# Performance work log

Hardware: AMD Instinct MI355X
Metric: run time of the kernel (lower is better)

The kernel has to match this reference:

```python
import jax, jax.numpy as jnp
import numpy as np

DIM = 768
HEADS = 12
T_TOK = 4  # num_frames // tubelet_size
EPS = 1e-6


def _layernorm(x, w, b):
    m = jnp.mean(x, axis=-1, keepdims=True)
    v = jnp.var(x, axis=-1, keepdims=True)
    return (x - m) * jax.lax.rsqrt(v + EPS) * w + b


def _conv1d(g, w, b):
    # g: (Bv, C, T), w: (C_out, C_in, 3) torch layout, padding=1
    y = jax.lax.conv_general_dilated(g, w, window_strides=(1,), padding=[(1, 1)],
                                     dimension_numbers=("NCH", "OIH", "NCH"))
    return y + b[None, :, None]


def setup_inputs() -> dict:
    key = jax.random.key(0)
    ks = jax.random.split(key, 16)
    D, F = DIM, DIM * 4
    s = 0.02
    return {
        "x": jax.random.normal(ks[0], (64, 197, D), jnp.float32),
        "ln1_w": jnp.ones((D,), jnp.float32),
        "ln1_b": jnp.zeros((D,), jnp.float32),
        "qkv_w": jax.random.normal(ks[1], (3 * D, D), jnp.float32) * s,
        "qkv_b": jnp.zeros((3 * D,), jnp.float32),
        "convq_w": jax.random.normal(ks[2], (D, D, 3), jnp.float32) * s,
        "convq_b": jnp.zeros((D,), jnp.float32),
        "convk_w": jax.random.normal(ks[3], (D, D, 3), jnp.float32) * s,
        "convk_b": jnp.zeros((D,), jnp.float32),
        "proj_w": jax.random.normal(ks[4], (D, D), jnp.float32) * s,
        "proj_b": jnp.zeros((D,), jnp.float32),
        "ln2_w": jnp.ones((D,), jnp.float32),
        "ln2_b": jnp.zeros((D,), jnp.float32),
        "ff1_w": jax.random.normal(ks[5], (F, D), jnp.float32) * s,
        "ff1_b": jnp.zeros((F,), jnp.float32),
        "ff2_w": jax.random.normal(ks[6], (D, F), jnp.float32) * s,
        "ff2_b": jnp.zeros((D,), jnp.float32),
    }


def reference(x, ln1_w, ln1_b, qkv_w, qkv_b, convq_w, convq_b, convk_w, convk_b,
              proj_w, proj_b, ln2_w, ln2_b, ff1_w, ff1_b, ff2_w, ff2_b):
    B, N, C = x.shape
    H, Dh = HEADS, C // HEADS

    # --- attention branch ---
    h = _layernorm(x, ln1_w, ln1_b)
    # temporal context from per-frame CLS tokens
    g = h[:, 0, :].reshape(B // T_TOK, T_TOK, C).transpose(0, 2, 1)  # (Bv, C, T)
    cq = _conv1d(g, convq_w, convq_b).transpose(0, 2, 1).reshape(B, H, 1, Dh)
    ck = _conv1d(g, convk_w, convk_b).transpose(0, 2, 1).reshape(B, H, 1, Dh)

    qkv = (h @ qkv_w.T + qkv_b).reshape(B, N, 3, H, Dh).transpose(2, 0, 3, 1, 4)
    q, k, v = qkv[0], qkv[1], qkv[2]  # (B, H, N, Dh)

    scale = Dh ** -0.5
    scores = jnp.einsum("bhnd,bhmd->bhnm", q + cq, k + ck) * scale
    attn = jax.nn.softmax(scores, axis=-1)
    o = jnp.einsum("bhnm,bhmd->bhnd", attn, v)
    o = o.transpose(0, 2, 1, 3).reshape(B, N, C)
    o = o @ proj_w.T + proj_b
    x = x + o

    # --- FFN branch ---
    h2 = _layernorm(x, ln2_w, ln2_b)
    h2 = jax.nn.gelu(h2 @ ff1_w.T + ff1_b, approximate=False)
    x = x + (h2 @ ff2_w.T + ff2_b)
    return x
```

## Files before the change

kernel.cpp:

```cpp
#include <hip/hip_runtime.h>
#include <hip/hip_bf16.h>


typedef __attribute__((ext_vector_type(8))) short  short8;
typedef __attribute__((ext_vector_type(4))) float  float4v;
typedef __attribute__((ext_vector_type(4))) unsigned short ushort4v;

#define DEV static __device__ __forceinline__

DEV unsigned short f2bf(float f) {
  union { float f; unsigned u; } v; v.f = f;
  unsigned r = v.u + 0x7fffu + ((v.u >> 16) & 1u);
  return (unsigned short)(r >> 16);
}
DEV float bf2f(unsigned short h) {
  union { unsigned u; float f; } v; v.u = ((unsigned)h) << 16;
  return v.f;
}

DEV void gld_lds16(const void* g, void* l) {
  __builtin_amdgcn_global_load_lds(
      (const __attribute__((address_space(1))) void*)g,
      (__attribute__((address_space(3))) void*)l, 16, 0, 0);
}

__global__ void wcvt(const float* __restrict__ in, unsigned short* __restrict__ out, int n4) {
  int i = blockIdx.x * 256 + threadIdx.x;
  if (i >= n4) return;
  float4 f = *((const float4*)in + i);
  ushort4v o;
  o[0] = f2bf(f.x); o[1] = f2bf(f.y); o[2] = f2bf(f.z); o[3] = f2bf(f.w);
  *(ushort4v*)(out + (size_t)i * 4) = o;
}

__global__ __launch_bounds__(256) void ln_k(const float* __restrict__ x,
                                            const float* __restrict__ w,
                                            const float* __restrict__ b,
                                            unsigned short* __restrict__ out) {
  int row = blockIdx.x;
  size_t base = (size_t)row * 768;
  int tid = threadIdx.x;
  float v0 = x[base + tid], v1 = x[base + tid + 256], v2 = x[base + tid + 512];
  float s = v0 + v1 + v2;
  float q = v0 * v0 + v1 * v1 + v2 * v2;
  for (int m = 1; m < 64; m <<= 1) { s += __shfl_xor(s, m); q += __shfl_xor(q, m); }
  __shared__ float sh[8];
  int wid = tid >> 6, lane = tid & 63;
  if (lane == 0) { sh[wid] = s; sh[4 + wid] = q; }
  __syncthreads();
  s = sh[0] + sh[1] + sh[2] + sh[3];
  q = sh[4] + sh[5] + sh[6] + sh[7];
  float mean = s * (1.f / 768.f);
  float var  = q * (1.f / 768.f) - mean * mean;
  float rstd = rsqrtf(var + 1e-6f);
  out[base + tid      ] = f2bf((v0 - mean) * rstd * w[tid      ] + b[tid      ]);
  out[base + tid + 256] = f2bf((v1 - mean) * rstd * w[tid + 256] + b[tid + 256]);
  out[base + tid + 512] = f2bf((v2 - mean) * rstd * w[tid + 512] + b[tid + 512]);
}

__global__ __launch_bounds__(256) void conv_cls(const unsigned short* __restrict__ h,
                                                const float* __restrict__ wq,
                                                const float* __restrict__ wk,
                                                float* __restrict__ cq,
                                                float* __restrict__ ck) {
  __shared__ float gsh[16][6][48];
  int tid = threadIdx.x;
  int cc = blockIdx.x;
  int kc = blockIdx.y;
  for (int idx = tid; idx < 16 * 2 * 48; idx += 256) {
    int ci = idx % 48; int t = (idx / 48) & 1; int v = idx / 96;
    gsh[v][t * 5][ci] = 0.f;
  }
  for (int idx = tid; idx < 16 * 4 * 48; idx += 256) {
    int ci = idx % 48; int t = (idx / 48) & 3; int v = idx / 192;
    gsh[v][t + 1][ci] = bf2f(h[(size_t)(v * 4 + t) * 197 * 768 + kc * 48 + ci]);
  }
  __syncthreads();
  int cl = tid >> 2, t = tid & 3;
  int cout = cc * 64 + cl;
  const float* wqp = wq + ((size_t)cout * 768 + kc * 48) * 3;
  const float* wkp = wk + ((size_t)cout * 768 + kc * 48) * 3;
  float aq[16] = {}, ak[16] = {};
  for (int ci = 0; ci < 48; ++ci) {
    float q0 = wqp[ci * 3], q1 = wqp[ci * 3 + 1], q2 = wqp[ci * 3 + 2];
    float k0 = wkp[ci * 3], k1 = wkp[ci * 3 + 1], k2 = wkp[ci * 3 + 2];
#pragma unroll
    for (int v = 0; v < 16; ++v) {
      float g0 = gsh[v][t][ci], g1 = gsh[v][t + 1][ci], g2 = gsh[v][t + 2][ci];
      aq[v] += q0 * g0 + q1 * g1 + q2 * g2;
      ak[v] += k0 * g0 + k1 * g1 + k2 * g2;
    }
  }
#pragma unroll
  for (int v = 0; v < 16; ++v) {
    atomicAdd(&cq[(size_t)(v * 4 + t) * 768 + cout], aq[v]);
    atomicAdd(&ck[(size_t)(v * 4 + t) * 768 + cout], ak[v]);
  }
}

template <int EPI>
__global__ __launch_bounds__(256, 2) void gemm_k(
    const unsigned short* __restrict__ A, const unsigned short* __restrict__ W,
    int M, int N, int K, const float* __restrict__ bias,
    float* __restrict__ out_f, unsigned short* __restrict__ out_h,
    const float* __restrict__ res,
    const float* __restrict__ cq, const float* __restrict__ ck,
    const float* __restrict__ cqb, const float* __restrict__ ckb,
    unsigned short* __restrict__ Qo, unsigned short* __restrict__ Ko,
    unsigned short* __restrict__ Vo) {
  __shared__ unsigned short As[128 * 32];
  __shared__ unsigned short Bs[128 * 32];
  int tid = threadIdx.x;
  int wid = tid >> 6, lane = tid & 63;
  int wr = wid >> 1, wc = wid & 1;
  int cG = lane >> 4, cl = lane & 15;
  long rowBase = (long)blockIdx.x * 128;
  int colBase = blockIdx.y * 128;

  float4v acc[4][4] = {};

  int off0 = tid * 16, off1 = (256 + tid) * 16;
  int r0s = off0 >> 6, r1s = off1 >> 6;
  int s0 = (off0 >> 4) & 3, s1 = (off1 >> 4) & 3;
  int k0s = (s0 ^ ((r0s >> 1) & 3)) * 8;
  int k1s = (s1 ^ ((r1s >> 1) & 3)) * 8;
  long ar0 = rowBase + r0s; if (ar0 > M - 1) ar0 = M - 1;
  long ar1 = rowBase + r1s; if (ar1 > M - 1) ar1 = M - 1;
  const unsigned short* a0 = A + ar0 * K + k0s;
  const unsigned short* a1 = A + ar1 * K + k1s;
  const unsigned short* w0 = W + (long)(colBase + r0s) * K + k0s;
  const unsigned short* w1 = W + (long)(colBase + r1s) * K + k1s;

  for (int kt = 0; kt < K; kt += 32) {
    __syncthreads();
    gld_lds16(a0 + kt, As + (off0 >> 1));
    gld_lds16(a1 + kt, As + (off1 >> 1));
    gld_lds16(w0 + kt, Bs + (off0 >> 1));
    gld_lds16(w1 + kt, Bs + (off1 >> 1));
    __syncthreads();
    short8 af[4], bfr[4];
#pragma unroll
    for (int fi = 0; fi < 4; ++fi) {
      int r = wr * 64 + fi * 16 + cl;
      int sl = cG ^ ((r >> 1) & 3);
      af[fi] = *(const short8*)(As + r * 32 + sl * 8);
    }
#pragma unroll
    for (int fj = 0; fj < 4; ++fj) {
      int r = wc * 64 + fj * 16 + cl;
      int sl = cG ^ ((r >> 1) & 3);
      bfr[fj] = *(const short8*)(Bs + r * 32 + sl * 8);
    }
#pragma unroll
    for (int fi = 0; fi < 4; ++fi)
#pragma unroll
      for (int fj = 0; fj < 4; ++fj)
        acc[fi][fj] = __builtin_amdgcn_mfma_f32_16x16x32_bf16(af[fi], bfr[fj], acc[fi][fj], 0, 0, 0);
  }

#pragma unroll
  for (int fi = 0; fi < 4; ++fi) {
    long r0 = rowBase + wr * 64 + fi * 16 + 4 * cG;
#pragma unroll
    for (int fj = 0; fj < 4; ++fj) {
      int col = colBase + wc * 64 + fj * 16 + cl;
      float bc = bias[col];
      float4v a = acc[fi][fj];
#pragma unroll
      for (int j = 0; j < 4; ++j) {
        long row = r0 + j;
        if (row >= M) continue;
        float v = a[j] + bc;
        if constexpr (EPI == 0) {
          int sec = col / 768; int ccc = col - sec * 768;
          int bi = (int)(row / 197); int ni = (int)(row - (long)bi * 197);
          size_t oidx = ((size_t)(bi * 12 + (ccc >> 6)) * 197 + ni) * 64 + (ccc & 63);
          if (sec == 0)      { v += cq[bi * 768 + ccc] + cqb[ccc]; Qo[oidx] = f2bf(v); }
          else if (sec == 1) { v += ck[bi * 768 + ccc] + ckb[ccc]; Ko[oidx] = f2bf(v); }
          else               { Vo[oidx] = f2bf(v); }
        } else if constexpr (EPI == 1 || EPI == 3) {
          size_t idx = (size_t)row * N + col;
          out_f[idx] = v + res[idx];
        } else {
          size_t idx = (size_t)row * N + col;
          float g = 0.5f * v * (1.0f + erff(v * 0.70710678118f));
          out_h[idx] = f2bf(g);
        }
      }
    }
  }
}

__global__ __launch_bounds__(256, 2) void attn_k(const unsigned short* __restrict__ Q,
                                                 const unsigned short* __restrict__ Kg,
                                                 const unsigned short* __restrict__ Vg,
                                                 unsigned short* __restrict__ O) {
  __shared__ unsigned short Ks[224 * 64];
  __shared__ unsigned short Vt[64 * 224];
  __shared__ unsigned short Ps[4][16 * 40];
  int g = blockIdx.x;
  int bi = g / 12, hh = g - bi * 12;
  size_t gbase = (size_t)g * 197 * 64;
  int tid = threadIdx.x, wid = tid >> 6, lane = tid & 63;
  int cG = lane >> 4, cl = lane & 15;

  {
    int rr = tid >> 3, ch = tid & 7;
#pragma unroll
    for (int i = 0; i < 7; ++i) {
      int n = rr + 32 * i;
      short8 kv = {0, 0, 0, 0, 0, 0, 0, 0};
      if (n < 197) kv = *(const short8*)(Kg + gbase + (size_t)n * 64 + ch * 8);
      *(short8*)(Ks + n * 64 + (ch ^ (n & 7)) * 8) = kv;
      short8 vv = {0, 0, 0, 0, 0, 0, 0, 0};
      if (n < 197) vv = *(const short8*)(Vg + gbase + (size_t)n * 64 + ch * 8);
#pragma unroll
      for (int j = 0; j < 8; ++j) {
        int dd = ch * 8 + j;
        Vt[dd * 224 + (n ^ ((dd & 7) << 3))] = ((unsigned short*)&vv)[j];
      }
    }
  }
  __syncthreads();

  for (int rt = wid; rt < 13; rt += 4) {
    int nq = rt * 16 + cl; if (nq > 196) nq = 196;
    short8 aq0 = *(const short8*)(Q + gbase + (size_t)nq * 64 + 8 * cG);
    short8 aq1 = *(const short8*)(Q + gbase + (size_t)nq * 64 + 32 + 8 * cG);
    float4v s[14];
#pragma unroll
    for (int ct = 0; ct < 14; ++ct) {
      float4v a = {0.f, 0.f, 0.f, 0.f};
      int np = ct * 16 + cl;
      short8 b0 = *(const short8*)(Ks + np * 64 + ((cG    ) ^ (np & 7)) * 8);
      short8 b1 = *(const short8*)(Ks + np * 64 + ((4 + cG) ^ (np & 7)) * 8);
      a = __builtin_amdgcn_mfma_f32_16x16x32_bf16(aq0, b0, a, 0, 0, 0);
      a = __builtin_amdgcn_mfma_f32_16x16x32_bf16(aq1, b1, a, 0, 0, 0);
      s[ct] = a;
    }
    float mx[4] = {-1e30f, -1e30f, -1e30f, -1e30f};
#pragma unroll
    for (int ct = 0; ct < 14; ++ct) {
      int colv = ct * 16 + cl;
#pragma unroll
      for (int j = 0; j < 4; ++j) {
        float v = (colv < 197) ? s[ct][j] * 0.125f : -1e30f;
        s[ct][j] = v;
        mx[j] = fmaxf(mx[j], v);
      }
    }
#pragma unroll
    for (int m = 1; m < 16; m <<= 1)
#pragma unroll
      for (int j = 0; j < 4; ++j) mx[j] = fmaxf(mx[j], __shfl_xor(mx[j], m));
    float sum[4] = {0.f, 0.f, 0.f, 0.f};
#pragma unroll
    for (int ct = 0; ct < 14; ++ct)
#pragma unroll
      for (int j = 0; j < 4; ++j) {
        float p = __expf(s[ct][j] - mx[j]);
        s[ct][j] = p;
        sum[j] += p;
      }
#pragma unroll
    for (int m = 1; m < 16; m <<= 1)
#pragma unroll
      for (int j = 0; j < 4; ++j) sum[j] += __shfl_xor(sum[j], m);
    float rs[4];
#pragma unroll
    for (int j = 0; j < 4; ++j) rs[j] = 1.0f / sum[j];

    float4v oa[4] = {};
    unsigned short* P = &Ps[wid][0];
#pragma unroll
    for (int ks = 0; ks < 7; ++ks) {
#pragma unroll
      for (int t = 0; t < 2; ++t) {
        int ct = 2 * ks + t;
#pragma unroll
        for (int j = 0; j < 4; ++j)
          P[(4 * cG + j) * 40 + t * 16 + cl] = f2bf(s[ct][j]);
      }
      short8 pa = *(const short8*)(P + cl * 40 + 8 * cG);
#pragma unroll
      for (int dt = 0; dt < 4; ++dt) {
        int dd = dt * 16 + cl;
        short8 bv = *(const short8*)(Vt + dd * 224 + ((ks * 32 + 8 * cG) ^ ((dd & 7) << 3)));
        oa[dt] = __builtin_amdgcn_mfma_f32_16x16x32_bf16(pa, bv, oa[dt], 0, 0, 0);
      }
    }
#pragma unroll
    for (int dt = 0; dt < 4; ++dt)
#pragma unroll
      for (int j = 0; j < 4; ++j) {
        int n2 = rt * 16 + 4 * cG + j;
        if (n2 < 197)
          O[(size_t)(bi * 197 + n2) * 768 + hh * 64 + dt * 16 + cl] = f2bf(oa[dt][j] * rs[j]);
      }
  }
}

extern "C" void kernel_launch(void* const* d_in, const int* in_sizes, int n_in,
                              void* d_out, int out_size, void* d_ws, size_t ws_size,
                              hipStream_t stream) {
  const float* x     = (const float*)d_in[0];
  const float* ln1w  = (const float*)d_in[1];
  const float* ln1b  = (const float*)d_in[2];
  const float* qkvw  = (const float*)d_in[3];
  const float* qkvb  = (const float*)d_in[4];
  const float* cqw   = (const float*)d_in[5];
  const float* cqb   = (const float*)d_in[6];
  const float* ckw   = (const float*)d_in[7];
  const float* ckb   = (const float*)d_in[8];
  const float* projw = (const float*)d_in[9];
  const float* projb = (const float*)d_in[10];
  const float* ln2w  = (const float*)d_in[11];
  const float* ln2b  = (const float*)d_in[12];
  const float* ff1w  = (const float*)d_in[13];
  const float* ff1b  = (const float*)d_in[14];
  const float* ff2w  = (const float*)d_in[15];
  const float* ff2b  = (const float*)d_in[16];
  float* out = (float*)d_out;

  char* ws = (char*)d_ws;
  const size_t SZ = (size_t)12608 * 768 * 2;
  unsigned short* Qb  = (unsigned short*)(ws);
  unsigned short* Kb  = (unsigned short*)(ws + SZ);
  unsigned short* Vb  = (unsigned short*)(ws + 2 * SZ);
  unsigned short* Ob  = (unsigned short*)(ws + 3 * SZ);
  unsigned short* ffh = (unsigned short*)(ws);
  unsigned short* hb  = (unsigned short*)(ws + 4 * SZ);
  float* x1 = (float*)(ws + 5 * SZ);
  float* cq = (float*)(ws + 5 * SZ + (size_t)12608 * 768 * 4);
  float* ck = cq + 49152;
  unsigned short* Wqkv  = (unsigned short*)(ck + 49152);
  unsigned short* Wproj = Wqkv + 1769472;
  unsigned short* Wff1  = Wproj + 589824;
  unsigned short* Wff2  = Wff1 + 2359296;

  wcvt<<<1728, 256, 0, stream>>>(qkvw, Wqkv, 442368);
  wcvt<<<576,  256, 0, stream>>>(projw, Wproj, 147456);
  wcvt<<<2304, 256, 0, stream>>>(ff1w, Wff1, 589824);
  wcvt<<<2304, 256, 0, stream>>>(ff2w, Wff2, 589824);

  ln_k<<<12608, 256, 0, stream>>>(x, ln1w, ln1b, hb);

  hipMemsetAsync(cq, 0, 2 * 49152 * sizeof(float), stream);
  conv_cls<<<dim3(12, 16), 256, 0, stream>>>(hb, cqw, ckw, cq, ck);

  gemm_k<0><<<dim3(99, 18), 256, 0, stream>>>(hb, Wqkv, 12608, 2304, 768, qkvb,
      nullptr, nullptr, nullptr, cq, ck, cqb, ckb, Qb, Kb, Vb);

  attn_k<<<768, 256, 0, stream>>>(Qb, Kb, Vb, Ob);

  gemm_k<1><<<dim3(99, 6), 256, 0, stream>>>(Ob, Wproj, 12608, 768, 768, projb,
      x1, nullptr, x, nullptr, nullptr, nullptr, nullptr, nullptr, nullptr, nullptr);

  ln_k<<<12608, 256, 0, stream>>>(x1, ln2w, ln2b, hb);

  gemm_k<2><<<dim3(99, 24), 256, 0, stream>>>(hb, Wff1, 12608, 3072, 768, ff1b,
      nullptr, ffh, nullptr, nullptr, nullptr, nullptr, nullptr, nullptr, nullptr, nullptr);

  gemm_k<3><<<dim3(99, 6), 256, 0, stream>>>(ffh, Wff2, 12608, 768, 3072, ff2b,
      out, nullptr, x1, nullptr, nullptr, nullptr, nullptr, nullptr, nullptr, nullptr);
}
```

Measured before the change: 624.5 us.

## Use 256x256 double-buffered GEMM tiles with XCD-aware scheduling and per-wave layernorm

The GEMM kernel goes from 128x128 tiles with K-step 32 and a single LDS buffer to 256x256 tiles with K-step 64 and double-buffered LDS, run by 512-thread blocks with 8 waves. The next tile is prefetched while the current one is multiplied, which removes one barrier per iteration and raises data reuse per load. Blocks are remapped by XCD so that neighbouring tiles share L2. LayerNorm now handles one row per wave with float4 loads and no shared-memory reduction. The cost is fewer blocks (150 for the N=768 GEMMs), which risks leaving CUs idle, plus 128KB of LDS per block, which likely limits occupancy to one block per CU despite launch_bounds(512,2).

```diff
diff --git a/kernel.cpp b/kernel.cpp
--- a/kernel.cpp
+++ b/kernel.cpp
@@ -5,15 +5,16 @@
 typedef __attribute__((ext_vector_type(8))) short  short8;
 typedef __attribute__((ext_vector_type(4))) float  float4v;
 typedef __attribute__((ext_vector_type(4))) unsigned short ushort4v;
+typedef unsigned short ushort;
 
 #define DEV static __device__ __forceinline__
 
-DEV unsigned short f2bf(float f) {
+DEV ushort f2bf(float f) {
   union { float f; unsigned u; } v; v.f = f;
   unsigned r = v.u + 0x7fffu + ((v.u >> 16) & 1u);
-  return (unsigned short)(r >> 16);
-}
-DEV float bf2f(unsigned short h) {
+  return (ushort)(r >> 16);
+}
+DEV float bf2f(ushort h) {
   union { unsigned u; float f; } v; v.u = ((unsigned)h) << 16;
   return v.f;
 }
@@ -24,7 +25,7 @@
       (__attribute__((address_space(3))) void*)l, 16, 0, 0);
 }
 
-__global__ void wcvt(const float* __restrict__ in, unsigned short* __restrict__ out, int n4) {
+__global__ void wcvt(const float* __restrict__ in, ushort* __restrict__ out, int n4) {
   int i = blockIdx.x * 256 + threadIdx.x;
   if (i >= n4) return;
   float4 f = *((const float4*)in + i);
@@ -36,29 +37,40 @@
 __global__ __launch_bounds__(256) void ln_k(const float* __restrict__ x,
                                             const float* __restrict__ w,
                                             const float* __restrict__ b,
-                                            unsigned short* __restrict__ out) {
-  int row = blockIdx.x;
+                                            ushort* __restrict__ out) {
+  int wid = threadIdx.x >> 6, lane = threadIdx.x & 63;
+  int row = blockIdx.x * 4 + wid;
   size_t base = (size_t)row * 768;
-  int tid = threadIdx.x;
-  float v0 = x[base + tid], v1 = x[base + tid + 256], v2 = x[base + tid + 512];
-  float s = v0 + v1 + v2;
-  float q = v0 * v0 + v1 * v1 + v2 * v2;
+  const float4* xr = (const float4*)(x + base);
+  const float4* w4 = (const float4*)w;
+  const float4* b4 = (const float4*)b;
+  float4 v[3];
+  float s = 0.f, q = 0.f;
+#pragma unroll
+  for (int j = 0; j < 3; ++j) {
+    v[j] = xr[j * 64 + lane];
+    s += v[j].x + v[j].y + v[j].z + v[j].w;
+    q += v[j].x * v[j].x + v[j].y * v[j].y + v[j].z * v[j].z + v[j].w * v[j].w;
+  }
+#pragma unroll
   for (int m = 1; m < 64; m <<= 1) { s += __shfl_xor(s, m); q += __shfl_xor(q, m); }
-  __shared__ float sh[8];
-  int wid = tid >> 6, lane = tid & 63;
-  if (lane == 0) { sh[wid] = s; sh[4 + wid] = q; }
-  __syncthreads();
-  s = sh[0] + sh[1] + sh[2] + sh[3];
-  q = sh[4] + sh[5] + sh[6] + sh[7];
   float mean = s * (1.f / 768.f);
   float var  = q * (1.f / 768.f) - mean * mean;
   float rstd = rsqrtf(var + 1e-6f);
-  out[base + tid      ] = f2bf((v0 - mean) * rstd * w[tid      ] + b[tid      ]);
-  out[base + tid + 256] = f2bf((v1 - mean) * rstd * w[tid + 256] + b[tid + 256]);
-  out[base + tid + 512] = f2bf((v2 - mean) * rstd * w[tid + 512] + b[tid + 512]);
-}
-
-__global__ __launch_bounds__(256) void conv_cls(const unsigned short* __restrict__ h,
+  ushort* orow = out + base;
+#pragma unroll
+  for (int j = 0; j < 3; ++j) {
+    float4 wv = w4[j * 64 + lane], bv = b4[j * 64 + lane];
+    ushort4v o;
+    o[0] = f2bf((v[j].x - mean) * rstd * wv.x + bv.x);
+    o[1] = f2bf((v[j].y - mean) * rstd * wv.y + bv.y);
+    o[2] = f2bf((v[j].z - mean) * rstd * wv.z + bv.z);
+    o[3] = f2bf((v[j].w - mean) * rstd * wv.w + bv.w);
+    *(ushort4v*)(orow + (size_t)(j * 64 + lane) * 4) = o;
+  }
+}
+
+__global__ __launch_bounds__(256) void conv_cls(const ushort* __restrict__ h,
                                                 const float* __restrict__ wq,
                                                 const float* __restrict__ wk,
                                                 float* __restrict__ cq,
@@ -99,68 +111,92 @@
 }
 
 template <int EPI>
-__global__ __launch_bounds__(256, 2) void gemm_k(
-    const unsigned short* __restrict__ A, const unsigned short* __restrict__ W,
-    int M, int N, int K, const float* __restrict__ bias,
-    float* __restrict__ out_f, unsigned short* __restrict__ out_h,
+__global__ __launch_bounds__(512, 2) void gemm256(
+    const ushort* __restrict__ A, const ushort* __restrict__ W,
+    int M, int N, int K, int mt, const float* __restrict__ bias,
+    float* __restrict__ out_f, ushort* __restrict__ out_h,
     const float* __restrict__ res,
     const float* __restrict__ cq, const float* __restrict__ ck,
     const float* __restrict__ cqb, const float* __restrict__ ckb,
-    unsigned short* __restrict__ Qo, unsigned short* __restrict__ Ko,
-    unsigned short* __restrict__ Vo) {
-  __shared__ unsigned short As[128 * 32];
-  __shared__ unsigned short Bs[128 * 32];
+    ushort* __restrict__ Qo, ushort* __restrict__ Ko, ushort* __restrict__ Vo) {
+  __shared__ ushort As[2][256 * 64];
+  __shared__ ushort Bs[2][256 * 64];
+
+  int nwg = gridDim.x;
+  int bid = blockIdx.x;
+  int q8 = nwg >> 3, r8 = nwg & 7;
+  int xcd = bid & 7, idx = bid >> 3;
+  int wg = (xcd < r8 ? xcd * (q8 + 1) : r8 * (q8 + 1) + (xcd - r8) * q8) + idx;
+  int tileCol = wg / mt;
+  int tileRow = wg - tileCol * mt;
+
+  long rowBase = (long)tileRow * 256;
+  int  colBase = tileCol * 256;
+
   int tid = threadIdx.x;
   int wid = tid >> 6, lane = tid & 63;
-  int wr = wid >> 1, wc = wid & 1;
+  int wr = wid >> 2, wc = wid & 3;
   int cG = lane >> 4, cl = lane & 15;
-  long rowBase = (long)blockIdx.x * 128;
-  int colBase = blockIdx.y * 128;
-
-  float4v acc[4][4] = {};
-
-  int off0 = tid * 16, off1 = (256 + tid) * 16;
-  int r0s = off0 >> 6, r1s = off1 >> 6;
-  int s0 = (off0 >> 4) & 3, s1 = (off1 >> 4) & 3;
-  int k0s = (s0 ^ ((r0s >> 1) & 3)) * 8;
-  int k1s = (s1 ^ ((r1s >> 1) & 3)) * 8;
-  long ar0 = rowBase + r0s; if (ar0 > M - 1) ar0 = M - 1;
-  long ar1 = rowBase + r1s; if (ar1 > M - 1) ar1 = M - 1;
-  const unsigned short* a0 = A + ar0 * K + k0s;
-  const unsigned short* a1 = A + ar1 * K + k1s;
-  const unsigned short* w0 = W + (long)(colBase + r0s) * K + k0s;
-  const unsigned short* w1 = W + (long)(colBase + r1s) * K + k1s;
-
-  for (int kt = 0; kt < K; kt += 32) {
+
+  const ushort* asrc[4];
+  const ushort* wsrc[4];
+  int dstoff[4];
+#pragma unroll
+  for (int j = 0; j < 4; ++j) {
+    int flat = j * 512 + tid;
+    int r = flat >> 3, c = flat & 7;
+    long ar = rowBase + r; if (ar > M - 1) ar = M - 1;
+    asrc[j] = A + ar * (size_t)K + (c ^ (r & 7)) * 8;
+    wsrc[j] = W + (size_t)(colBase + r) * K + (c ^ (r & 7)) * 8;
+    dstoff[j] = flat * 8;
+  }
+
+  float4v acc[8][4] = {};
+
+#pragma unroll
+  for (int j = 0; j < 4; ++j) {
+    gld_lds16(asrc[j], &As[0][0] + dstoff[j]);
+    gld_lds16(wsrc[j], &Bs[0][0] + dstoff[j]);
+  }
+  __syncthreads();
+
+  int nt = K >> 6;
+  for (int t = 0; t < nt; ++t) {
+    const ushort* as = &As[t & 1][0];
+    const ushort* bs = &Bs[t & 1][0];
+    if (t + 1 < nt) {
+      ushort* an = &As[(t + 1) & 1][0];
+      ushort* bn = &Bs[(t + 1) & 1][0];
+      int kt = (t + 1) << 6;
+#pragma unroll
+      for (int j = 0; j < 4; ++j) {
+        gld_lds16(asrc[j] + kt, an + dstoff[j]);
+        gld_lds16(wsrc[j] + kt, bn + dstoff[j]);
+      }
+    }
+#pragma unroll
+    for (int ks = 0; ks < 2; ++ks) {
+      short8 bfv[4];
+#pragma unroll
+      for (int fj = 0; fj < 4; ++fj) {
+        int r = wc * 64 + fj * 16 + cl;
+        bfv[fj] = *(const short8*)(bs + r * 64 + (((ks << 2) | cG) ^ (r & 7)) * 8);
+      }
+#pragma unroll
+      for (int fi = 0; fi < 8; ++fi) {
+        int r = wr * 128 + fi * 16 + cl;
+        short8 av = *(const short8*)(as + r * 64 + (((ks << 2) | cG) ^ (r & 7)) * 8);
+#pragma unroll
+        for (int fj = 0; fj < 4; ++fj)
+          acc[fi][fj] = __builtin_amdgcn_mfma_f32_16x16x32_bf16(av, bfv[fj], acc[fi][fj], 0, 0, 0);
+      }
+    }
     __syncthreads();
-    gld_lds16(a0 + kt, As + (off0 >> 1));
-    gld_lds16(a1 + kt, As + (off1 >> 1));
-    gld_lds16(w0 + kt, Bs + (off0 >> 1));
-    gld_lds16(w1 + kt, Bs + (off1 >> 1));
-    __syncthreads();
-    short8 af[4], bfr[4];
-#pragma unroll
-    for (int fi = 0; fi < 4; ++fi) {
-      int r = wr * 64 + fi * 16 + cl;
-      int sl = cG ^ ((r >> 1) & 3);
-      af[fi] = *(const short8*)(As + r * 32 + sl * 8);
-    }
-#pragma unroll
-    for (int fj = 0; fj < 4; ++fj) {
-      int r = wc * 64 + fj * 16 + cl;
-      int sl = cG ^ ((r >> 1) & 3);
-      bfr[fj] = *(const short8*)(Bs + r * 32 + sl * 8);
-    }
-#pragma unroll
-    for (int fi = 0; fi < 4; ++fi)
-#pragma unroll
-      for (int fj = 0; fj < 4; ++fj)
-        acc[fi][fj] = __builtin_amdgcn_mfma_f32_16x16x32_bf16(af[fi], bfr[fj], acc[fi][fj], 0, 0, 0);
-  }
-
-#pragma unroll
-  for (int fi = 0; fi < 4; ++fi) {
-    long r0 = rowBase + wr * 64 + fi * 16 + 4 * cG;
+  }
+
+#pragma unroll
+  for (int fi = 0; fi < 8; ++fi) {
+    long r0 = rowBase + wr * 128 + fi * 16 + 4 * cG;
 #pragma unroll
     for (int fj = 0; fj < 4; ++fj) {
       int col = colBase + wc * 64 + fj * 16 + cl;
@@ -191,13 +227,13 @@
   }
 }
 
-__global__ __launch_bounds__(256, 2) void attn_k(const unsigned short* __restrict__ Q,
-                                                 const unsigned short* __restrict__ Kg,
-                                                 const unsigned short* __restrict__ Vg,
-                                                 unsigned short* __restrict__ O) {
-  __shared__ unsigned short Ks[224 * 64];
-  __shared__ unsigned short Vt[64 * 224];
-  __shared__ unsigned short Ps[4][16 * 40];
+__global__ __launch_bounds__(256, 2) void attn_k(const ushort* __restrict__ Q,
+                                                 const ushort* __restrict__ Kg,
+                                                 const ushort* __restrict__ Vg,
+                                                 ushort* __restrict__ O) {
+  __shared__ ushort Ks[224 * 64];
+  __shared__ ushort Vt[64 * 224];
+  __shared__ ushort Ps[4][16 * 40];
   int g = blockIdx.x;
   int bi = g / 12, hh = g - bi * 12;
   size_t gbase = (size_t)g * 197 * 64;
@@ -217,7 +253,7 @@
 #pragma unroll
       for (int j = 0; j < 8; ++j) {
         int dd = ch * 8 + j;
-        Vt[dd * 224 + (n ^ ((dd & 7) << 3))] = ((unsigned short*)&vv)[j];
+        Vt[dd * 224 + (n ^ ((dd & 7) << 3))] = ((ushort*)&vv)[j];
       }
     }
   }
@@ -271,7 +307,7 @@
     for (int j = 0; j < 4; ++j) rs[j] = 1.0f / sum[j];
 
     float4v oa[4] = {};
-    unsigned short* P = &Ps[wid][0];
+    ushort* P = &Ps[wid][0];
 #pragma unroll
     for (int ks = 0; ks < 7; ++ks) {
 #pragma unroll
@@ -324,43 +360,43 @@
 
   char* ws = (char*)d_ws;
   const size_t SZ = (size_t)12608 * 768 * 2;
-  unsigned short* Qb  = (unsigned short*)(ws);
-  unsigned short* Kb  = (unsigned short*)(ws + SZ);
-  unsigned short* Vb  = (unsigned short*)(ws + 2 * SZ);
-  unsigned short* Ob  = (unsigned short*)(ws + 3 * SZ);
-  unsigned short* ffh = (unsigned short*)(ws);
-  unsigned short* hb  = (unsigned short*)(ws + 4 * SZ);
+  ushort* Qb  = (ushort*)(ws);
+  ushort* Kb  = (ushort*)(ws + SZ);
+  ushort* Vb  = (ushort*)(ws + 2 * SZ);
+  ushort* Ob  = (ushort*)(ws + 3 * SZ);
+  ushort* ffh = (ushort*)(ws);
+  ushort* hb  = (ushort*)(ws + 4 * SZ);
   float* x1 = (float*)(ws + 5 * SZ);
   float* cq = (float*)(ws + 5 * SZ + (size_t)12608 * 768 * 4);
   float* ck = cq + 49152;
-  unsigned short* Wqkv  = (unsigned short*)(ck + 49152);
-  unsigned short* Wproj = Wqkv + 1769472;
-  unsigned short* Wff1  = Wproj + 589824;
-  unsigned short* Wff2  = Wff1 + 2359296;
+  ushort* Wqkv  = (ushort*)(ck + 49152);
+  ushort* Wproj = Wqkv + 1769472;
+  ushort* Wff1  = Wproj + 589824;
+  ushort* Wff2  = Wff1 + 2359296;
 
   wcvt<<<1728, 256, 0, stream>>>(qkvw, Wqkv, 442368);
   wcvt<<<576,  256, 0, stream>>>(projw, Wproj, 147456);
   wcvt<<<2304, 256, 0, stream>>>(ff1w, Wff1, 589824);
   wcvt<<<2304, 256, 0, stream>>>(ff2w, Wff2, 589824);
 
-  ln_k<<<12608, 256, 0, stream>>>(x, ln1w, ln1b, hb);
+  ln_k<<<3152, 256, 0, stream>>>(x, ln1w, ln1b, hb);
 
   hipMemsetAsync(cq, 0, 2 * 49152 * sizeof(float), stream);
   conv_cls<<<dim3(12, 16), 256, 0, stream>>>(hb, cqw, ckw, cq, ck);
 
-  gemm_k<0><<<dim3(99, 18), 256, 0, stream>>>(hb, Wqkv, 12608, 2304, 768, qkvb,
+  gemm256<0><<<450, 512, 0, stream>>>(hb, Wqkv, 12608, 2304, 768, 50, qkvb,
       nullptr, nullptr, nullptr, cq, ck, cqb, ckb, Qb, Kb, Vb);
 
   attn_k<<<768, 256, 0, stream>>>(Qb, Kb, Vb, Ob);
 
-  gemm_k<1><<<dim3(99, 6), 256, 0, stream>>>(Ob, Wproj, 12608, 768, 768, projb,
+  gemm256<1><<<150, 512, 0, stream>>>(Ob, Wproj, 12608, 768, 768, 50, projb,
       x1, nullptr, x, nullptr, nullptr, nullptr, nullptr, nullptr, nullptr, nullptr);
 
-  ln_k<<<12608, 256, 0, stream>>>(x1, ln2w, ln2b, hb);
-
-  gemm_k<2><<<dim3(99, 24), 256, 0, stream>>>(hb, Wff1, 12608, 3072, 768, ff1b,
+  ln_k<<<3152, 256, 0, stream>>>(x1, ln2w, ln2b, hb);
+
+  gemm256<2><<<600, 512, 0, stream>>>(hb, Wff1, 12608, 3072, 768, 50, ff1b,
       nullptr, ffh, nullptr, nullptr, nullptr, nullptr, nullptr, nullptr, nullptr, nullptr);
 
-  gemm_k<3><<<dim3(99, 6), 256, 0, stream>>>(ffh, Wff2, 12608, 768, 3072, ff2b,
+  gemm256<3><<<150, 512, 0, stream>>>(ffh, Wff2, 12608, 768, 3072, 50, ff2b,
       out, nullptr, x1, nullptr, nullptr, nullptr, nullptr, nullptr, nullptr, nullptr);
 }
```

Result: slower. 697.4 us (+11.7%).
